# Performance work log

Measured on AMD Instinct MI355X. Metric: run time of the kernel, lower is better.

## Reference

```python
import jax, jax.numpy as jnp
import numpy as np

NEG = -1000000.0

def setup_inputs() -> dict:
    key = jax.random.key(0)
    ks = jax.random.split(key, 7)
    B, Lq, Lk, Dq, Dk, Dv, H = 4, 256, 1024, 512, 512, 512, 256
    return {
        "query": jax.random.normal(ks[0], (B, Lq, Dq), dtype=jnp.float32),
        "key": jax.random.normal(ks[1], (B, Lk, Dk), dtype=jnp.float32),
        "value": jax.random.normal(ks[2], (B, Lk, Dv), dtype=jnp.float32),
        "valid_len": jax.random.randint(ks[3], (B,), 1, Lk + 1),
        "Wq": jax.random.normal(ks[4], (Dq, H), dtype=jnp.float32) * (1.0 / np.sqrt(Dq)),
        "Wk": jax.random.normal(ks[5], (Dk, H), dtype=jnp.float32) * (1.0 / np.sqrt(Dk)),
        "wv": jax.random.normal(ks[6], (H,), dtype=jnp.float32) * (1.0 / np.sqrt(H)),
    }

def reference(query, key, value, valid_len, Wq, Wk, wv):
    # projections: [B,Lq,H], [B,Lk,H]
    q = jnp.einsum("bqd,dh->bqh", query, Wq)
    k = jnp.einsum("bkd,dh->bkh", key, Wk)
    # broadcast-add + tanh: [B,Lq,Lk,H]
    features = jnp.tanh(q[:, :, None, :] + k[:, None, :, :])
    # score projection to scalar: [B,Lq,Lk]
    score = jnp.einsum("bqkh,h->bqk", features, wv)
    # masked softmax over keys (valid_len per batch, broadcast over queries)
    Lk = key.shape[1]
    mask = jnp.arange(Lk)[None, None, :] < valid_len[:, None, None]
    score = jnp.where(mask, score, NEG)
    attn = jax.nn.softmax(score, axis=-1)
    # weighted sum of values: [B,Lq,Dv]  (dropout is identity in eval)
    return jnp.einsum("bqk,bkv->bqv", attn, value)
```

## Files before the change

### kernel.cpp

```cpp
#include <hip/hip_runtime.h>

typedef __attribute__((ext_vector_type(8))) short short8v;
typedef __attribute__((ext_vector_type(4))) float float4v;
typedef unsigned int uint;

#define TWO_LOG2E 2.8853900817779268f
#define LOG2E     1.4426950408889634f

__device__ inline uint rne_bf16(float x) {
    uint u = __float_as_uint(x);
    return (u + 0x7fffu + ((u >> 16) & 1u)) >> 16;
}
__device__ inline uint pack_hi_lo(float a0, float a1, uint& lo_pack) {
    const uint h0 = rne_bf16(a0), h1 = rne_bf16(a1);
    const float f0 = __uint_as_float(h0 << 16), f1 = __uint_as_float(h1 << 16);
    const float l0 = a0 - f0, l1 = a1 - f1;
    lo_pack = (rne_bf16(l1) << 16) | rne_bf16(l0);
    return (h1 << 16) | h0;
}

__global__ __launch_bounds__(256) void prep_a(
    const float* __restrict__ query, const float* __restrict__ key,
    const int* __restrict__ vlen,
    ushort* __restrict__ A_hi, ushort* __restrict__ A_lo)
{
    const int t = blockIdx.x * 256 + threadIdx.x;
    const int row = t >> 6;
    const int cg = (t & 63) * 8;
    if (row >= 1024) {
        const int kr = (row - 1024) & 1023, b = (row - 1024) >> 10;
        if ((kr & ~63) >= vlen[b]) return;
    }
    const float* src = (row < 1024) ? (query + (size_t)row * 512 + cg)
                                    : (key + (size_t)(row - 1024) * 512 + cg);
    const float4 x0 = *(const float4*)src;
    const float4 x1 = *(const float4*)(src + 4);
    uint h0, h1, h2, h3, l0, l1, l2, l3;
    h0 = pack_hi_lo(x0.x, x0.y, l0);
    h1 = pack_hi_lo(x0.z, x0.w, l1);
    h2 = pack_hi_lo(x1.x, x1.y, l2);
    h3 = pack_hi_lo(x1.z, x1.w, l3);
    *(uint4*)(A_hi + (size_t)row * 512 + cg) = make_uint4(h0, h1, h2, h3);
    *(uint4*)(A_lo + (size_t)row * 512 + cg) = make_uint4(l0, l1, l2, l3);
}

__global__ __launch_bounds__(256) void prep_w(
    const float* __restrict__ Wq, const float* __restrict__ Wk,
    ushort* __restrict__ WT_hi, ushort* __restrict__ WT_lo)
{
    const int t = blockIdx.x * 256 + threadIdx.x;
    const int n = t & 255;
    const int kg = ((t >> 8) & 63) * 8;
    const int w = t >> 14;
    const float* W = w ? Wk : Wq;
    float x[8];
    #pragma unroll
    for (int i = 0; i < 8; ++i) x[i] = W[(size_t)(kg + i) * 256 + n];
    uint h0, h1, h2, h3, l0, l1, l2, l3;
    h0 = pack_hi_lo(x[0], x[1], l0);
    h1 = pack_hi_lo(x[2], x[3], l1);
    h2 = pack_hi_lo(x[4], x[5], l2);
    h3 = pack_hi_lo(x[6], x[7], l3);
    const size_t off = ((size_t)w * 256 + n) * 512 + kg;
    *(uint4*)(WT_hi + off) = make_uint4(h0, h1, h2, h3);
    *(uint4*)(WT_lo + off) = make_uint4(l0, l1, l2, l3);
}

__global__ __launch_bounds__(256) void prep_v(
    const float* __restrict__ value, const int* __restrict__ vlen,
    ushort* __restrict__ VT_hi, ushort* __restrict__ VT_lo)
{
    __shared__ float t[64][69];
    const int b = blockIdx.z;
    const int k0 = blockIdx.y * 64, n0 = blockIdx.x * 64;
    const int kendB = (vlen[b] + 31) & ~31;
    if (k0 >= kendB) return;

    const int tid = threadIdx.x;
    const int n_in = (tid & 15) * 4, k_in = tid >> 4;
    const float* src = value + ((size_t)b * 1024 + k0 + k_in) * 512 + n0 + n_in;
    #pragma unroll
    for (int p = 0; p < 4; ++p) {
        const float4 x = *(const float4*)(src + (size_t)p * 16 * 512);
        t[k_in + p * 16][n_in + 0] = x.x;
        t[k_in + p * 16][n_in + 1] = x.y;
        t[k_in + p * 16][n_in + 2] = x.z;
        t[k_in + p * 16][n_in + 3] = x.w;
    }
    __syncthreads();

    const int rn = tid >> 2, c0 = (tid & 3) * 16;
    uint hp[8], lp[8];
    #pragma unroll
    for (int i = 0; i < 8; ++i)
        hp[i] = pack_hi_lo(t[c0 + 2 * i][rn], t[c0 + 2 * i + 1][rn], lp[i]);
    const size_t off = ((size_t)b * 512 + n0 + rn) * 1024 + k0 + c0;
    *(uint4*)(VT_hi + off) = make_uint4(hp[0], hp[1], hp[2], hp[3]);
    *(uint4*)(VT_hi + off + 8) = make_uint4(hp[4], hp[5], hp[6], hp[7]);
    *(uint4*)(VT_lo + off) = make_uint4(lp[0], lp[1], lp[2], lp[3]);
    *(uint4*)(VT_lo + off + 8) = make_uint4(lp[4], lp[5], lp[6], lp[7]);
}

#define LOADF(s, kbase) { const int ko = (kbase) + half * 8;                \
    _Pragma("unroll") for (int f = 0; f < 2; ++f) {                         \
        ah##s[f] = *(const short8v*)(a_h + (size_t)(f * 16) * 512 + ko);    \
        al##s[f] = *(const short8v*)(a_l + (size_t)(f * 16) * 512 + ko); }  \
    _Pragma("unroll") for (int f = 0; f < 4; ++f) {                         \
        bh##s[f] = *(const short8v*)(wt_h + (size_t)(f * 16) * 512 + ko);   \
        bl##s[f] = *(const short8v*)(wt_l + (size_t)(f * 16) * 512 + ko); } }

#define MFMAS(s)                                                                          \
    _Pragma("unroll") for (int mf = 0; mf < 2; ++mf)                                      \
    _Pragma("unroll") for (int nf = 0; nf < 4; ++nf) {                                    \
        acc[mf][nf] = __builtin_amdgcn_mfma_f32_16x16x32_bf16(ah##s[mf], bh##s[nf], acc[mf][nf], 0, 0, 0); \
        acc[mf][nf] = __builtin_amdgcn_mfma_f32_16x16x32_bf16(ah##s[mf], bl##s[nf], acc[mf][nf], 0, 0, 0); \
        acc[mf][nf] = __builtin_amdgcn_mfma_f32_16x16x32_bf16(al##s[mf], bh##s[nf], acc[mf][nf], 0, 0, 0); }

__global__ __launch_bounds__(64) void proj_mfma(
    const ushort* __restrict__ A_hi, const ushort* __restrict__ A_lo,
    const ushort* __restrict__ WT_hi, const ushort* __restrict__ WT_lo,
    const int* __restrict__ valid_len,
    float* __restrict__ EqT, float* __restrict__ EkT)
{
    const int lane = threadIdx.x;
    const int n0 = blockIdx.x * 64;
    const int m0 = blockIdx.y * 32;
    const bool isq = (m0 < 1024);
    int b = 0, kk0 = 0;
    if (!isq) {
        kk0 = (m0 - 1024) & 1023;
        b = (m0 - 1024) >> 10;
        if (kk0 >= valid_len[b]) return;
    }
    const int r = lane & 15, half = lane >> 4;
    const size_t wsel = isq ? 0 : (size_t)256 * 512;
    const ushort* wt_h = WT_hi + wsel + (size_t)(n0 + r) * 512;
    const ushort* wt_l = WT_lo + wsel + (size_t)(n0 + r) * 512;
    const ushort* a_h = A_hi + (size_t)(m0 + r) * 512;
    const ushort* a_l = A_lo + (size_t)(m0 + r) * 512;

    float4v acc[2][4] = {{{0.f}}};
    short8v ah0[2], al0[2], bh0[4], bl0[4];
    short8v ah1[2], al1[2], bh1[4], bl1[4];

    LOADF(0, 0);
    for (int kt = 0; kt < 512; kt += 64) {
        LOADF(1, kt + 32);
        MFMAS(0);
        if (kt + 64 < 512) LOADF(0, kt + 64);
        MFMAS(1);
    }

    #pragma unroll
    for (int mf = 0; mf < 2; ++mf) {
        #pragma unroll
        for (int nf = 0; nf < 4; ++nf) {
            float4v e;
            #pragma unroll
            for (int i = 0; i < 4; ++i)
                e[i] = __builtin_amdgcn_exp2f(acc[mf][nf][i] * TWO_LOG2E);
            if (isq) {
                *(float4v*)(EqT + (size_t)(n0 + nf * 16 + r) * 1024 +
                            m0 + mf * 16 + half * 4) = e;
            } else {
                *(float4v*)(EkT + (size_t)(b * 256 + n0 + nf * 16 + r) * 1024 +
                            kk0 + mf * 16 + half * 4) = e;
            }
        }
    }
}

__global__ __launch_bounds__(256) void score_partial(
    const float* __restrict__ EqT, const float* __restrict__ EkT,
    const float* __restrict__ wv, const int* __restrict__ valid_len,
    float* __restrict__ P)
{
    __shared__ float eqs[64][8];
    __shared__ float wvs[64];

    const int idx = blockIdx.x;
    const int hq = idx & 3;
    const int kt = (idx >> 2) & 3;
    const int qg = (idx >> 4) & 31;
    const int b  = idx >> 9;

    const int vlen = valid_len[b];
    if (kt * 256 >= vlen) return;

    const int tid = threadIdx.x;
    const int k = kt * 256 + tid;
    const int q0 = qg * 8;
    const int h0 = hq * 64;

    if (tid < 64) wvs[tid] = wv[h0 + tid];
    #pragma unroll
    for (int r = 0; r < 2; ++r) {
        const int i = r * 256 + tid;
        const int h = i >> 3, q = i & 7;
        eqs[h][q] = EqT[(size_t)(h0 + h) * 1024 + b * 256 + q0 + q];
    }
    __syncthreads();

    float acc[8] = {};
    if (k < vlen) {
        const float* ekp = EkT + (size_t)(b * 256 + h0) * 1024 + k;
        #pragma unroll 2
        for (int h = 0; h < 64; ++h) {
            const float ek = ekp[(size_t)h * 1024];
            const float w = wvs[h];
            const float4 e0 = *(const float4*)&eqs[h][0];
            const float4 e1 = *(const float4*)&eqs[h][4];
            acc[0] = fmaf(w, __builtin_amdgcn_rcpf(fmaf(e0.x, ek, 1.f)), acc[0]);
            acc[1] = fmaf(w, __builtin_amdgcn_rcpf(fmaf(e0.y, ek, 1.f)), acc[1]);
            acc[2] = fmaf(w, __builtin_amdgcn_rcpf(fmaf(e0.z, ek, 1.f)), acc[2]);
            acc[3] = fmaf(w, __builtin_amdgcn_rcpf(fmaf(e0.w, ek, 1.f)), acc[3]);
            acc[4] = fmaf(w, __builtin_amdgcn_rcpf(fmaf(e1.x, ek, 1.f)), acc[4]);
            acc[5] = fmaf(w, __builtin_amdgcn_rcpf(fmaf(e1.y, ek, 1.f)), acc[5]);
            acc[6] = fmaf(w, __builtin_amdgcn_rcpf(fmaf(e1.z, ek, 1.f)), acc[6]);
            acc[7] = fmaf(w, __builtin_amdgcn_rcpf(fmaf(e1.w, ek, 1.f)), acc[7]);
        }
    }

    float* Pq = P + (size_t)hq * 1048576;
    #pragma unroll
    for (int qi = 0; qi < 8; ++qi)
        Pq[(size_t)(b * 256 + q0 + qi) * 1024 + k] = acc[qi];
}

__global__ __launch_bounds__(1024) void softmax_kernel(
    const float* __restrict__ P, const int* __restrict__ valid_len,
    ushort* __restrict__ attn_hi, ushort* __restrict__ attn_lo)
{
    __shared__ float red[16][4];

    const int tid = threadIdx.x;
    const int b = blockIdx.x >> 6;
    const int q0 = (blockIdx.x & 63) << 2;

    const int vlen = valid_len[b];
    const int k = tid;
    const bool v = (k < vlen);

    float s[4], m[4];
    #pragma unroll
    for (int q = 0; q < 4; ++q) {
        const size_t off = (size_t)(b * 256 + q0 + q) * 1024 + k;
        s[q] = -2.f * (P[off] + P[off + 1048576] +
                       P[off + 2097152] + P[off + 3145728]);
        m[q] = v ? s[q] : -1e30f;
    }
    #pragma unroll
    for (int o = 32; o; o >>= 1) {
        #pragma unroll
        for (int q = 0; q < 4; ++q) m[q] = fmaxf(m[q], __shfl_xor(m[q], o));
    }
    const int wid = tid >> 6;
    if ((tid & 63) == 0) {
        #pragma unroll
        for (int q = 0; q < 4; ++q) red[wid][q] = m[q];
    }
    __syncthreads();
    #pragma unroll
    for (int q = 0; q < 4; ++q) {
        float mm = red[0][q];
        #pragma unroll
        for (int w = 1; w < 16; ++w) mm = fmaxf(mm, red[w][q]);
        m[q] = mm;
    }
    __syncthreads();

    float p[4], l[4];
    #pragma unroll
    for (int q = 0; q < 4; ++q) {
        p[q] = v ? __builtin_amdgcn_exp2f((s[q] - m[q]) * LOG2E) : 0.f;
        l[q] = p[q];
    }
    #pragma unroll
    for (int o = 32; o; o >>= 1) {
        #pragma unroll
        for (int q = 0; q < 4; ++q) l[q] += __shfl_xor(l[q], o);
    }
    if ((tid & 63) == 0) {
        #pragma unroll
        for (int q = 0; q < 4; ++q) red[wid][q] = l[q];
    }
    __syncthreads();
    #pragma unroll
    for (int q = 0; q < 4; ++q) {
        float ss = red[0][q];
        #pragma unroll
        for (int w = 1; w < 16; ++w) ss += red[w][q];
        const float a = p[q] * __builtin_amdgcn_rcpf(ss);
        const uint hi = rne_bf16(a);
        const float lo = a - __uint_as_float(hi << 16);
        const size_t off = (size_t)(b * 256 + q0 + q) * 1024 + k;
        attn_hi[off] = (ushort)hi;
        attn_lo[off] = (ushort)rne_bf16(lo);
    }
}

#define PVLOAD(s, ko) {                                   \
    ah##s = *(const short8v*)(ah_p + (ko));               \
    al##s = *(const short8v*)(al_p + (ko));               \
    bh0##s = *(const short8v*)(bh_p + (ko));              \
    bl0##s = *(const short8v*)(bl_p + (ko));              \
    bh1##s = *(const short8v*)(bh_p + 16 * 1024 + (ko));  \
    bl1##s = *(const short8v*)(bl_p + 16 * 1024 + (ko)); }

#define PVMFMA(s) {                                                              \
    acc0 = __builtin_amdgcn_mfma_f32_16x16x32_bf16(ah##s, bh0##s, acc0, 0, 0, 0); \
    acc0 = __builtin_amdgcn_mfma_f32_16x16x32_bf16(ah##s, bl0##s, acc0, 0, 0, 0); \
    acc0 = __builtin_amdgcn_mfma_f32_16x16x32_bf16(al##s, bh0##s, acc0, 0, 0, 0); \
    acc1 = __builtin_amdgcn_mfma_f32_16x16x32_bf16(ah##s, bh1##s, acc1, 0, 0, 0); \
    acc1 = __builtin_amdgcn_mfma_f32_16x16x32_bf16(ah##s, bl1##s, acc1, 0, 0, 0); \
    acc1 = __builtin_amdgcn_mfma_f32_16x16x32_bf16(al##s, bh1##s, acc1, 0, 0, 0); }

__global__ __launch_bounds__(64) void pv_mfma(
    const ushort* __restrict__ attn_hi, const ushort* __restrict__ attn_lo,
    const ushort* __restrict__ VT_hi, const ushort* __restrict__ VT_lo,
    const int* __restrict__ valid_len,
    float* __restrict__ out)
{
    const int lane = threadIdx.x;
    const int n0 = blockIdx.x * 32;
    const int q0 = blockIdx.y * 16;
    const int b = blockIdx.z;
    const int r = lane & 15, half = lane >> 4;
    const int kend = (valid_len[b] + 31) & ~31;

    const ushort* ah_p = attn_hi + (size_t)(b * 256 + q0 + r) * 1024 + half * 8;
    const ushort* al_p = attn_lo + (size_t)(b * 256 + q0 + r) * 1024 + half * 8;
    const ushort* bh_p = VT_hi + (size_t)(b * 512 + n0 + r) * 1024 + half * 8;
    const ushort* bl_p = VT_lo + (size_t)(b * 512 + n0 + r) * 1024 + half * 8;

    float4v acc0 = {0.f}, acc1 = {0.f};
    short8v ah0, al0, bh00, bl00, bh10, bl10;
    short8v ah1, al1, bh01, bl01, bh11, bl11;

    PVLOAD(0, 0);
    for (int kt = 0; kt < kend; kt += 64) {
        if (kt + 32 < kend) PVLOAD(1, kt + 32);
        PVMFMA(0);
        if (kt + 64 < kend) PVLOAD(0, kt + 64);
        if (kt + 32 < kend) PVMFMA(1);
    }

    float* op = out + (size_t)b * 256 * 512 + (size_t)(q0 + half * 4) * 512 + n0 + r;
    #pragma unroll
    for (int i = 0; i < 4; ++i) {
        op[(size_t)i * 512] = acc0[i];
        op[(size_t)i * 512 + 16] = acc1[i];
    }
}

extern "C" void kernel_launch(void* const* d_in, const int* in_sizes, int n_in,
                              void* d_out, int out_size, void* d_ws, size_t ws_size,
                              hipStream_t stream)
{
    const float* query = (const float*)d_in[0];
    const float* key   = (const float*)d_in[1];
    const float* value = (const float*)d_in[2];
    const int*   vlen  = (const int*)d_in[3];
    const float* Wq    = (const float*)d_in[4];
    const float* Wk    = (const float*)d_in[5];
    const float* wv    = (const float*)d_in[6];
    float* out = (float*)d_out;

    float*  EqT     = (float*)d_ws;
    float*  EkT     = EqT + 262144;
    float*  P       = EkT + 1048576;
    ushort* A_hi    = (ushort*)(P + 4194304);
    ushort* A_lo    = A_hi + 2621440;
    ushort* WT_hi   = A_lo + 2621440;
    ushort* WT_lo   = WT_hi + 262144;
    ushort* attn_hi = WT_lo + 262144;
    ushort* attn_lo = attn_hi + 1048576;
    ushort* VT_hi   = attn_lo + 1048576;
    ushort* VT_lo   = VT_hi + 2097152;

    hipLaunchKernelGGL(prep_w, dim3(128), dim3(256), 0, stream,
                       Wq, Wk, WT_hi, WT_lo);
    hipLaunchKernelGGL(prep_a, dim3(1280), dim3(256), 0, stream,
                       query, key, vlen, A_hi, A_lo);
    hipLaunchKernelGGL(prep_v, dim3(8, 16, 4), dim3(256), 0, stream,
                       value, vlen, VT_hi, VT_lo);
    hipLaunchKernelGGL(proj_mfma, dim3(4, 160), dim3(64), 0, stream,
                       A_hi, A_lo, WT_hi, WT_lo, vlen, EqT, EkT);
    hipLaunchKernelGGL(score_partial, dim3(2048), dim3(256), 0, stream,
                       EqT, EkT, wv, vlen, P);
    hipLaunchKernelGGL(softmax_kernel, dim3(256), dim3(1024), 0, stream,
                       P, vlen, attn_hi, attn_lo);
    hipLaunchKernelGGL(pv_mfma, dim3(16, 16, 4), dim3(64), 0, stream,
                       attn_hi, attn_lo, VT_hi, VT_lo, vlen, out);
}
```

Baseline: 87.76 us.

## Fuse input bf16 split into projection, reduce head partials in LDS, regroup PV blocks

```diff
diff --git a/kernel.cpp b/kernel.cpp
--- a/kernel.cpp
+++ b/kernel.cpp
@@ -18,30 +18,17 @@
     lo_pack = (rne_bf16(l1) << 16) | rne_bf16(l0);
     return (h1 << 16) | h0;
 }
-
-__global__ __launch_bounds__(256) void prep_a(
-    const float* __restrict__ query, const float* __restrict__ key,
-    const int* __restrict__ vlen,
-    ushort* __restrict__ A_hi, ushort* __restrict__ A_lo)
-{
-    const int t = blockIdx.x * 256 + threadIdx.x;
-    const int row = t >> 6;
-    const int cg = (t & 63) * 8;
-    if (row >= 1024) {
-        const int kr = (row - 1024) & 1023, b = (row - 1024) >> 10;
-        if ((kr & ~63) >= vlen[b]) return;
-    }
-    const float* src = (row < 1024) ? (query + (size_t)row * 512 + cg)
-                                    : (key + (size_t)(row - 1024) * 512 + cg);
-    const float4 x0 = *(const float4*)src;
-    const float4 x1 = *(const float4*)(src + 4);
-    uint h0, h1, h2, h3, l0, l1, l2, l3;
-    h0 = pack_hi_lo(x0.x, x0.y, l0);
-    h1 = pack_hi_lo(x0.z, x0.w, l1);
-    h2 = pack_hi_lo(x1.x, x1.y, l2);
-    h3 = pack_hi_lo(x1.z, x1.w, l3);
-    *(uint4*)(A_hi + (size_t)row * 512 + cg) = make_uint4(h0, h1, h2, h3);
-    *(uint4*)(A_lo + (size_t)row * 512 + cg) = make_uint4(l0, l1, l2, l3);
+__device__ inline void split8(const float4 x0, const float4 x1,
+                              short8v& h, short8v& l) {
+    const float xs[8] = {x0.x, x0.y, x0.z, x0.w, x1.x, x1.y, x1.z, x1.w};
+    #pragma unroll
+    for (int j = 0; j < 8; ++j) {
+        const uint u = __float_as_uint(xs[j]);
+        const uint hi = u & 0xFFFF0000u;
+        const float lo = xs[j] - __uint_as_float(hi);
+        h[j] = (short)(hi >> 16);
+        l[j] = (short)rne_bf16(lo);
+    }
 }
 
 __global__ __launch_bounds__(256) void prep_w(
@@ -101,12 +88,15 @@
     *(uint4*)(VT_lo + off + 8) = make_uint4(lp[4], lp[5], lp[6], lp[7]);
 }
 
-#define LOADF(s, kbase) { const int ko = (kbase) + half * 8;                \
-    _Pragma("unroll") for (int f = 0; f < 2; ++f) {                         \
-        ah##s[f] = *(const short8v*)(a_h + (size_t)(f * 16) * 512 + ko);    \
-        al##s[f] = *(const short8v*)(a_l + (size_t)(f * 16) * 512 + ko); }  \
-    _Pragma("unroll") for (int f = 0; f < 4; ++f) {                         \
-        bh##s[f] = *(const short8v*)(wt_h + (size_t)(f * 16) * 512 + ko);   \
+#define LOADA(s, kbase) { const int ko = (kbase) + half * 8;                   \
+    _Pragma("unroll") for (int f = 0; f < 2; ++f) {                            \
+        const float4 x0 = *(const float4*)(a_f + (size_t)(f * 16) * 512 + ko); \
+        const float4 x1 = *(const float4*)(a_f + (size_t)(f * 16) * 512 + ko + 4); \
+        split8(x0, x1, ah##s[f], al##s[f]); } }
+
+#define LOADB(s, kbase) { const int ko = (kbase) + half * 8;                   \
+    _Pragma("unroll") for (int f = 0; f < 4; ++f) {                            \
+        bh##s[f] = *(const short8v*)(wt_h + (size_t)(f * 16) * 512 + ko);      \
         bl##s[f] = *(const short8v*)(wt_l + (size_t)(f * 16) * 512 + ko); } }
 
 #define MFMAS(s)                                                                          \
@@ -117,7 +107,7 @@
         acc[mf][nf] = __builtin_amdgcn_mfma_f32_16x16x32_bf16(al##s[mf], bh##s[nf], acc[mf][nf], 0, 0, 0); }
 
 __global__ __launch_bounds__(64) void proj_mfma(
-    const ushort* __restrict__ A_hi, const ushort* __restrict__ A_lo,
+    const float* __restrict__ query, const float* __restrict__ key,
     const ushort* __restrict__ WT_hi, const ushort* __restrict__ WT_lo,
     const int* __restrict__ valid_len,
     float* __restrict__ EqT, float* __restrict__ EkT)
@@ -136,18 +126,18 @@
     const size_t wsel = isq ? 0 : (size_t)256 * 512;
     const ushort* wt_h = WT_hi + wsel + (size_t)(n0 + r) * 512;
     const ushort* wt_l = WT_lo + wsel + (size_t)(n0 + r) * 512;
-    const ushort* a_h = A_hi + (size_t)(m0 + r) * 512;
-    const ushort* a_l = A_lo + (size_t)(m0 + r) * 512;
+    const float* a_f = isq ? (query + (size_t)(m0 + r) * 512)
+                           : (key + (size_t)(m0 - 1024 + r) * 512);
 
     float4v acc[2][4] = {{{0.f}}};
     short8v ah0[2], al0[2], bh0[4], bl0[4];
     short8v ah1[2], al1[2], bh1[4], bl1[4];
 
-    LOADF(0, 0);
+    LOADA(0, 0); LOADB(0, 0);
     for (int kt = 0; kt < 512; kt += 64) {
-        LOADF(1, kt + 32);
+        LOADA(1, kt + 32); LOADB(1, kt + 32);
         MFMAS(0);
-        if (kt + 64 < 512) LOADF(0, kt + 64);
+        if (kt + 64 < 512) { LOADA(0, kt + 64); LOADB(0, kt + 64); }
         MFMAS(1);
     }
 
@@ -170,46 +160,49 @@
     }
 }
 
-__global__ __launch_bounds__(256) void score_partial(
+__global__ __launch_bounds__(1024) void score_partial(
     const float* __restrict__ EqT, const float* __restrict__ EkT,
     const float* __restrict__ wv, const int* __restrict__ valid_len,
     float* __restrict__ P)
 {
-    __shared__ float eqs[64][8];
-    __shared__ float wvs[64];
-
-    const int idx = blockIdx.x;
-    const int hq = idx & 3;
-    const int kt = (idx >> 2) & 3;
-    const int qg = (idx >> 4) & 31;
-    const int b  = idx >> 9;
+    __shared__ float eqs[256][8];
+    __shared__ float wvs[256];
+    __shared__ float part[4][8][256];
+
+    const int orig = blockIdx.x;
+    const int wgid = (orig & 7) * 64 + (orig >> 3);
+    const int qg = wgid & 31;
+    const int rest = wgid >> 5;
+    const int kt = rest & 3;
+    const int b = rest >> 2;
 
     const int vlen = valid_len[b];
     if (kt * 256 >= vlen) return;
 
     const int tid = threadIdx.x;
-    const int k = kt * 256 + tid;
+    const int hq = tid >> 8, kl = tid & 255;
+    const int k = kt * 256 + kl;
     const int q0 = qg * 8;
-    const int h0 = hq * 64;
-
-    if (tid < 64) wvs[tid] = wv[h0 + tid];
-    #pragma unroll
-    for (int r = 0; r < 2; ++r) {
-        const int i = r * 256 + tid;
-        const int h = i >> 3, q = i & 7;
-        eqs[h][q] = EqT[(size_t)(h0 + h) * 1024 + b * 256 + q0 + q];
+
+    if (tid < 256) wvs[tid] = wv[tid];
+    {
+        const int i0 = tid * 2;
+        const int h = i0 >> 3, q = i0 & 7;
+        const float* ep = EqT + (size_t)h * 1024 + b * 256 + q0 + q;
+        eqs[h][q] = ep[0];
+        eqs[h][q + 1] = ep[1];
     }
     __syncthreads();
 
     float acc[8] = {};
     if (k < vlen) {
-        const float* ekp = EkT + (size_t)(b * 256 + h0) * 1024 + k;
+        const float* ekp = EkT + (size_t)(b * 256 + hq * 64) * 1024 + k;
         #pragma unroll 2
         for (int h = 0; h < 64; ++h) {
             const float ek = ekp[(size_t)h * 1024];
-            const float w = wvs[h];
-            const float4 e0 = *(const float4*)&eqs[h][0];
-            const float4 e1 = *(const float4*)&eqs[h][4];
+            const float w = wvs[hq * 64 + h];
+            const float4 e0 = *(const float4*)&eqs[hq * 64 + h][0];
+            const float4 e1 = *(const float4*)&eqs[hq * 64 + h][4];
             acc[0] = fmaf(w, __builtin_amdgcn_rcpf(fmaf(e0.x, ek, 1.f)), acc[0]);
             acc[1] = fmaf(w, __builtin_amdgcn_rcpf(fmaf(e0.y, ek, 1.f)), acc[1]);
             acc[2] = fmaf(w, __builtin_amdgcn_rcpf(fmaf(e0.z, ek, 1.f)), acc[2]);
@@ -221,10 +214,17 @@
         }
     }
 
-    float* Pq = P + (size_t)hq * 1048576;
-    #pragma unroll
-    for (int qi = 0; qi < 8; ++qi)
-        Pq[(size_t)(b * 256 + q0 + qi) * 1024 + k] = acc[qi];
+    #pragma unroll
+    for (int q = 0; q < 8; ++q) part[hq][q][kl] = acc[q];
+    __syncthreads();
+
+    #pragma unroll
+    for (int j = 0; j < 2; ++j) {
+        const int q = hq * 2 + j;
+        const float s = part[0][q][kl] + part[1][q][kl] +
+                        part[2][q][kl] + part[3][q][kl];
+        P[(size_t)(b * 256 + q0 + q) * 1024 + k] = -2.f * s;
+    }
 }
 
 __global__ __launch_bounds__(1024) void softmax_kernel(
@@ -244,9 +244,7 @@
     float s[4], m[4];
     #pragma unroll
     for (int q = 0; q < 4; ++q) {
-        const size_t off = (size_t)(b * 256 + q0 + q) * 1024 + k;
-        s[q] = -2.f * (P[off] + P[off + 1048576] +
-                       P[off + 2097152] + P[off + 3145728]);
+        s[q] = P[(size_t)(b * 256 + q0 + q) * 1024 + k];
         m[q] = v ? s[q] : -1e30f;
     }
     #pragma unroll
@@ -315,16 +313,22 @@
     acc1 = __builtin_amdgcn_mfma_f32_16x16x32_bf16(ah##s, bl1##s, acc1, 0, 0, 0); \
     acc1 = __builtin_amdgcn_mfma_f32_16x16x32_bf16(al##s, bh1##s, acc1, 0, 0, 0); }
 
-__global__ __launch_bounds__(64) void pv_mfma(
+__global__ __launch_bounds__(256) void pv_mfma(
     const ushort* __restrict__ attn_hi, const ushort* __restrict__ attn_lo,
     const ushort* __restrict__ VT_hi, const ushort* __restrict__ VT_lo,
     const int* __restrict__ valid_len,
     float* __restrict__ out)
 {
-    const int lane = threadIdx.x;
-    const int n0 = blockIdx.x * 32;
-    const int q0 = blockIdx.y * 16;
-    const int b = blockIdx.z;
+    const int orig = blockIdx.x;
+    const int wgid = (orig & 7) * 32 + (orig >> 3);
+    const int qb = wgid & 3;
+    const int rest = wgid >> 2;
+    const int b = rest & 3;
+    const int nt = rest >> 2;
+
+    const int wid = threadIdx.x >> 6, lane = threadIdx.x & 63;
+    const int n0 = nt * 32;
+    const int q0 = qb * 64 + wid * 16;
     const int r = lane & 15, half = lane >> 4;
     const int kend = (valid_len[b] + 31) & ~31;
 
@@ -369,9 +373,7 @@
     float*  EqT     = (float*)d_ws;
     float*  EkT     = EqT + 262144;
     float*  P       = EkT + 1048576;
-    ushort* A_hi    = (ushort*)(P + 4194304);
-    ushort* A_lo    = A_hi + 2621440;
-    ushort* WT_hi   = A_lo + 2621440;
+    ushort* WT_hi   = (ushort*)(P + 1048576);
     ushort* WT_lo   = WT_hi + 262144;
     ushort* attn_hi = WT_lo + 262144;
     ushort* attn_lo = attn_hi + 1048576;
@@ -380,16 +382,14 @@
 
     hipLaunchKernelGGL(prep_w, dim3(128), dim3(256), 0, stream,
                        Wq, Wk, WT_hi, WT_lo);
-    hipLaunchKernelGGL(prep_a, dim3(1280), dim3(256), 0, stream,
-                       query, key, vlen, A_hi, A_lo);
     hipLaunchKernelGGL(prep_v, dim3(8, 16, 4), dim3(256), 0, stream,
                        value, vlen, VT_hi, VT_lo);
     hipLaunchKernelGGL(proj_mfma, dim3(4, 160), dim3(64), 0, stream,
-                       A_hi, A_lo, WT_hi, WT_lo, vlen, EqT, EkT);
-    hipLaunchKernelGGL(score_partial, dim3(2048), dim3(256), 0, stream,
+                       query, key, WT_hi, WT_lo, vlen, EqT, EkT);
+    hipLaunchKernelGGL(score_partial, dim3(512), dim3(1024), 0, stream,
                        EqT, EkT, wv, vlen, P);
     hipLaunchKernelGGL(softmax_kernel, dim3(256), dim3(1024), 0, stream,
                        P, vlen, attn_hi, attn_lo);
-    hipLaunchKernelGGL(pv_mfma, dim3(16, 16, 4), dim3(64), 0, stream,
+    hipLaunchKernelGGL(pv_mfma, dim3(256), dim3(256), 0, stream,
                        attn_hi, attn_lo, VT_hi, VT_lo, vlen, out);
 }
```

After: 86.02 us. -2.0%, faster.
